# Performance work log

Hardware: AMD Instinct MI355X
Metric: run time of the kernel (lower is better)

The kernel has to match this reference:

```python
import jax, jax.numpy as jnp
import numpy as np
from jax import lax

B, S, D, H, TMAX = 8, 512, 256, 4, 20
DH = D // H
LAMBDA = 1e-3
V_TH = 1.0


def setup_inputs() -> dict:
    key = jax.random.key(0)
    ks = jax.random.split(key, 10)
    sc = lambda n: 1.0 / np.sqrt(n)
    f32 = jnp.float32
    return {
        "x": jax.random.normal(ks[0], (B, S, D), f32),
        "Wq": (jax.random.normal(ks[1], (D, D), f32) * sc(D)),
        "Wk": (jax.random.normal(ks[2], (D, D), f32) * sc(D)),
        "Wv": (jax.random.normal(ks[3], (D, D), f32) * sc(D)),
        "Wo": (jax.random.normal(ks[4], (D, D), f32) * sc(D)),
        "bo": jnp.zeros((D,), f32),
        "Wg1": (jax.random.normal(ks[5], (D, 32), f32) * sc(D)),
        "bg1": jnp.zeros((32,), f32),
        "Wg2": (jax.random.normal(ks[6], (32, 1), f32) * sc(32)),
        "bg2": jnp.zeros((1,), f32),
        "alpha_q": jnp.asarray(np.exp(-1 / 5.0), f32),
        "beta_q": jnp.asarray(np.exp(-1 / 20.0), f32),
        "alpha_k": jnp.asarray(np.exp(-1 / 5.0), f32),
        "beta_k": jnp.asarray(np.exp(-1 / 20.0), f32),
        "alpha_v": jnp.asarray(np.exp(-1 / 5.0), f32),
        "beta_v": jnp.asarray(np.exp(-1 / 20.0), f32),
    }


def _lif_spikes(x, alpha, beta, Ti):
    """LIF recurrence with CONSTANT input x per step, sequential only over T.
    x: [B,S,D], Ti: [B,S] int. Returns spikes [B,S,TMAX,D], zeroed for t >= Ti
    (equivalent to the original per-(b,s) loop that only runs Ti steps,
    since the recurrence is causal)."""
    zeros = jnp.zeros_like(x)
    tmask = jnp.arange(TMAX)

    def step(carry, t):
        v, i = carry
        i = alpha * i + x
        v = beta * v + i
        spk = (v >= V_TH).astype(x.dtype)
        v = v * (1.0 - spk)  # v_reset = 0
        spk_out = spk * (t < Ti).astype(x.dtype)[..., None]
        return (v, i), spk_out

    _, spks = lax.scan(step, (zeros, zeros), tmask)
    return jnp.moveaxis(spks, 0, 2)  # [B,S,T,D]


def reference(x, Wq, Wk, Wv, Wo, bo, Wg1, bg1, Wg2, bg2,
              alpha_q, beta_q, alpha_k, beta_k, alpha_v, beta_v):
    q = x @ Wq
    k = x @ Wk
    v = x @ Wv
    # adaptive window gate -> Ti in [1, TMAX]
    gate = jax.nn.sigmoid(jax.nn.relu(x @ Wg1 + bg1) @ Wg2 + bg2)[..., 0]  # [B,S]
    Ti = jnp.clip(jnp.ceil(gate * TMAX), 1, TMAX).astype(jnp.int32)
    q_spk = _lif_spikes(q, alpha_q, beta_q, Ti)  # [B,S,T,D]
    k_spk = _lif_spikes(k, alpha_k, beta_k, Ti)
    v_spk = _lif_spikes(v, alpha_v, beta_v, Ti)
    qh = q_spk.reshape(B, S, TMAX, H, DH)
    kh = k_spk.reshape(B, S, TMAX, H, DH)
    vh = v_spk.reshape(B, S, TMAX, H, DH)
    scale = DH ** -0.5
    Sraw = jnp.einsum('bithd,bjthd->bhij', qh, kh) * scale  # [B,H,S,S]
    W = jax.nn.softmax(Sraw, axis=-1)
    v_mean = vh.mean(axis=2)  # [B,S,H,DH] (mean over full T, zeros beyond Ti)
    out = jnp.einsum('bhij,bjhd->bihd', W, v_mean).reshape(B, S, D)
    out = out @ Wo + bo
    reg = LAMBDA * Ti.astype(jnp.float32).mean()
    return out, reg, Ti, W
```

## Files before the change

kernel.cpp:

```cpp
#include <hip/hip_runtime.h>
#include <hip/hip_bf16.h>

typedef unsigned long long u64;
typedef unsigned short u16;
typedef __attribute__((ext_vector_type(8))) short short8;
typedef __attribute__((ext_vector_type(4))) float float4_t;

#define BB 8
#define SS 512
#define DD 256
#define HH 4
#define TT 20
#define BS (BB*SS)

#define REG_OFF (BS*DD)
#define TI_OFF  (REG_OFF+1)
#define W_OFF   (TI_OFF+BS)

static __device__ __forceinline__ u16 f2bf(float f) {
    __hip_bfloat16 h = __float2bfloat16(f);
    return *reinterpret_cast<u16*>(&h);
}

__global__ __launch_bounds__(256) void k_gate(
    const float* __restrict__ x,
    const float* __restrict__ Wg1, const float* __restrict__ bg1,
    const float* __restrict__ Wg2, const float* __restrict__ bg2,
    float* __restrict__ ti_out)
{
    __shared__ float xl[8][DD];
    const int tid  = threadIdx.x;
    const int tok0 = blockIdx.x * 8;
    #pragma unroll
    for (int m = 0; m < 8; ++m) xl[m][tid] = x[(size_t)(tok0+m)*DD + tid];
    __syncthreads();

    const int tok = tid >> 5, c = tid & 31;
    float acc = bg1[c];
    #pragma unroll 4
    for (int r = 0; r < DD; ++r) acc += xl[tok][r] * Wg1[r*32 + c];
    float hrelu = acc > 0.f ? acc : 0.f;
    float term  = hrelu * Wg2[c];
    #pragma unroll
    for (int msk = 16; msk >= 1; msk >>= 1) term += __shfl_xor(term, msk, 64);
    if (c == 0) {
        float g  = term + bg2[0];
        float sg = 1.f / (1.f + expf(-g));
        int ti = (int)ceilf(sg * (float)TT);
        ti = ti < 1 ? 1 : (ti > TT ? TT : ti);
        ti_out[tok0 + tok] = (float)ti;
    }
}

__global__ __launch_bounds__(256) void k_proj_lif(
    const float* __restrict__ x, const float* __restrict__ Wq,
    const float* __restrict__ Wk, const float* __restrict__ Wv,
    const float* __restrict__ aq, const float* __restrict__ bq_,
    const float* __restrict__ ak, const float* __restrict__ bk_,
    const float* __restrict__ av, const float* __restrict__ bv_,
    const float* __restrict__ ti_in,
    u64* __restrict__ qpack, u64* __restrict__ kpack,
    u16* __restrict__ vmb)
{
    __shared__ float xl[DD][8];
    __shared__ int til[8];
    const int tid  = threadIdx.x;
    const int proj = blockIdx.y;
    const int tok0 = blockIdx.x * 8;

    #pragma unroll
    for (int m = 0; m < 8; ++m) xl[tid][m] = x[(size_t)(tok0+m)*DD + tid];
    if (tid < 8) til[tid] = (int)ti_in[tok0 + tid];
    __syncthreads();

    const float* W    = proj == 0 ? Wq  : (proj == 1 ? Wk  : Wv);
    const float alpha = proj == 0 ? *aq : (proj == 1 ? *ak : *av);
    const float beta  = proj == 0 ? *bq_: (proj == 1 ? *bk_: *bv_);

    float acc[8] = {0,0,0,0,0,0,0,0};
    #pragma unroll 4
    for (int r = 0; r < DD; ++r) {
        float w = W[r*DD + tid];
        float4_t x0 = *reinterpret_cast<const float4_t*>(&xl[r][0]);
        float4_t x1 = *reinterpret_cast<const float4_t*>(&xl[r][4]);
        acc[0] += x0.x*w; acc[1] += x0.y*w; acc[2] += x0.z*w; acc[3] += x0.w*w;
        acc[4] += x1.x*w; acc[5] += x1.y*w; acc[6] += x1.z*w; acc[7] += x1.w*w;
    }

    const int lane = tid & 63;
    const int h    = tid >> 6;
    u64* pack = (proj == 0) ? qpack : kpack;

    if (proj < 2) {
        for (int i = 0; i < 8; ++i) {
            int ti = til[i];
            float vv = 0.f, cur = 0.f;
            u64 myw = 0ull;
            #pragma unroll
            for (int t = 0; t < TT; ++t) {
                cur = alpha*cur + acc[i];
                vv  = beta*vv + cur;
                bool s = (vv >= 1.f);
                u64 bal = __ballot(s);
                if (s) vv = 0.f;
                if (lane == t && t < ti) myw = bal;
            }
            if (lane < TT) pack[((size_t)(tok0+i)*HH + h)*TT + lane] = myw;
        }
    } else {
        for (int i = 0; i < 8; ++i) {
            int ti = til[i];
            float vv = 0.f, cur = 0.f;
            float cnt = 0.f;
            #pragma unroll
            for (int t = 0; t < TT; ++t) {
                cur = alpha*cur + acc[i];
                vv  = beta*vv + cur;
                bool s = (vv >= 1.f);
                if (s) { vv = 0.f; if (t < ti) cnt += 1.f; }
            }
            vmb[(size_t)(tok0+i)*DD + tid] = f2bf(cnt * 0.05f);
        }
    }
}

__global__ __launch_bounds__(256) void k_reg(const float* __restrict__ ti, float* __restrict__ reg)
{
    __shared__ float ps[4];
    int tid = threadIdx.x;
    float s = 0.f;
    for (int m = 0; m < 16; ++m) s += ti[m*256 + tid];
    for (int msk = 32; msk >= 1; msk >>= 1) s += __shfl_xor(s, msk, 64);
    if ((tid & 63) == 0) ps[tid >> 6] = s;
    __syncthreads();
    if (tid == 0) reg[0] = 1e-3f * (ps[0]+ps[1]+ps[2]+ps[3]) / 4096.f;
}

__global__ __launch_bounds__(256) void k_attn(
    const u64* __restrict__ qpack, const u64* __restrict__ kpack,
    const u16* __restrict__ vmb,
    float* __restrict__ Wout, float* __restrict__ attn)
{
    __shared__ u64 ql[16][TT];
    __shared__ __align__(16) u16 CP[16*SS];
    const int tid  = threadIdx.x;
    const int tile = blockIdx.x & 31;
    const int h    = (blockIdx.x >> 5) & 3;
    const int b    = blockIdx.x >> 7;
    const int i0   = tile * 16;
    const int lane = tid & 63, wv = tid >> 6;

    for (int idx = tid; idx < 16*TT; idx += 256) {
        int i = idx / TT, t = idx - i*TT;
        ql[i][t] = qpack[((size_t)(b*SS + i0 + i)*HH + h)*TT + t];
    }

    u64 kr0[TT], kr1[TT];
    {
        const u64* kp0 = &kpack[((size_t)(b*SS + tid      )*HH + h)*TT];
        const u64* kp1 = &kpack[((size_t)(b*SS + tid + 256)*HH + h)*TT];
        #pragma unroll
        for (int t = 0; t < TT; ++t) { kr0[t] = kp0[t]; kr1[t] = kp1[t]; }
    }
    __syncthreads();

    for (int i = 0; i < 16; ++i) {
        int c0 = 0, c1 = 0;
        #pragma unroll
        for (int t = 0; t < TT; ++t) {
            u64 q = ql[i][t];
            c0 += __popcll(q & kr0[t]);
            c1 += __popcll(q & kr1[t]);
        }
        CP[i*SS + tid]       = (u16)c0;
        CP[i*SS + tid + 256] = (u16)c1;
    }
    __syncthreads();

    for (int rr = 0; rr < 4; ++rr) {
        const int i = wv*4 + rr;
        float sv[8];
        float m = -1e30f;
        #pragma unroll
        for (int k2 = 0; k2 < 8; ++k2) {
            sv[k2] = (float)CP[i*SS + lane + 64*k2] * 0.125f;
            m = fmaxf(m, sv[k2]);
        }
        #pragma unroll
        for (int msk = 32; msk >= 1; msk >>= 1) m = fmaxf(m, __shfl_xor(m, msk, 64));
        float sum = 0.f;
        #pragma unroll
        for (int k2 = 0; k2 < 8; ++k2) { sv[k2] = expf(sv[k2] - m); sum += sv[k2]; }
        #pragma unroll
        for (int msk = 32; msk >= 1; msk >>= 1) sum += __shfl_xor(sum, msk, 64);
        float inv = 1.f / sum;
        size_t wbase = ((size_t)((b*HH + h)*SS) + i0 + i) * SS;
        #pragma unroll
        for (int k2 = 0; k2 < 8; ++k2) {
            int j = lane + 64*k2;
            float wval = sv[k2] * inv;
            Wout[wbase + j] = wval;
            CP[(i*SS + j) ^ ((i & 7) << 3)] = f2bf(wval);
        }
    }
    __syncthreads();

    const int n0 = wv * 16;
    const int mr = lane & 15;
    const int g  = lane >> 4;
    float4_t acc = {0.f, 0.f, 0.f, 0.f};
    const u16* vb_base = vmb + (size_t)b*SS*DD + h*64 + n0 + mr;
    for (int ks = 0; ks < 16; ++ks) {
        int k = ks*32 + g*8;
        int aidx = (mr*SS + k) ^ ((mr & 7) << 3);
        short8 a = *reinterpret_cast<const short8*>(&CP[aidx]);
        union { u16 u[8]; short8 v; } bu;
        const u16* vb = vb_base + (size_t)k*DD;
        #pragma unroll
        for (int j = 0; j < 8; ++j) bu.u[j] = vb[(size_t)j*DD];
        acc = __builtin_amdgcn_mfma_f32_16x16x32_bf16(a, bu.v, acc, 0, 0, 0);
    }
    #pragma unroll
    for (int r = 0; r < 4; ++r) {
        int row = g*4 + r;
        attn[(size_t)(b*SS + i0 + row)*DD + h*64 + n0 + mr] = acc[r];
    }
}

__global__ __launch_bounds__(256) void k_outproj(
    const float* __restrict__ attn, const float* __restrict__ Wo,
    const float* __restrict__ bo, float* __restrict__ out)
{
    __shared__ float al[DD][8];
    const int tid  = threadIdx.x;
    const int tok0 = blockIdx.x * 8;
    #pragma unroll
    for (int m = 0; m < 8; ++m) al[tid][m] = attn[(size_t)(tok0+m)*DD + tid];
    __syncthreads();
    float acc[8] = {0,0,0,0,0,0,0,0};
    #pragma unroll 4
    for (int r = 0; r < DD; ++r) {
        float w = Wo[r*DD + tid];
        float4_t a0 = *reinterpret_cast<const float4_t*>(&al[r][0]);
        float4_t a1 = *reinterpret_cast<const float4_t*>(&al[r][4]);
        acc[0] += a0.x*w; acc[1] += a0.y*w; acc[2] += a0.z*w; acc[3] += a0.w*w;
        acc[4] += a1.x*w; acc[5] += a1.y*w; acc[6] += a1.z*w; acc[7] += a1.w*w;
    }
    float bb = bo[tid];
    #pragma unroll
    for (int i = 0; i < 8; ++i) out[(size_t)(tok0+i)*DD + tid] = acc[i] + bb;
}

extern "C" void kernel_launch(void* const* d_in, const int* in_sizes, int n_in,
                              void* d_out, int out_size, void* d_ws, size_t ws_size,
                              hipStream_t stream)
{
    (void)in_sizes; (void)n_in; (void)out_size; (void)ws_size;
    const float* x   = (const float*)d_in[0];
    const float* Wq  = (const float*)d_in[1];
    const float* Wk  = (const float*)d_in[2];
    const float* Wv  = (const float*)d_in[3];
    const float* Wo  = (const float*)d_in[4];
    const float* bo  = (const float*)d_in[5];
    const float* Wg1 = (const float*)d_in[6];
    const float* bg1 = (const float*)d_in[7];
    const float* Wg2 = (const float*)d_in[8];
    const float* bg2 = (const float*)d_in[9];
    const float* aq  = (const float*)d_in[10];
    const float* bq  = (const float*)d_in[11];
    const float* ak  = (const float*)d_in[12];
    const float* bk  = (const float*)d_in[13];
    const float* av  = (const float*)d_in[14];
    const float* bv  = (const float*)d_in[15];
    float* out = (float*)d_out;

    u64* qp = (u64*)d_ws;
    u64* kp = qp + (size_t)BS*HH*TT;
    u16* vmb = (u16*)(kp + (size_t)BS*HH*TT);
    float* attnbuf = (float*)(vmb + (size_t)BS*DD);

    k_gate<<<512, 256, 0, stream>>>(x, Wg1, bg1, Wg2, bg2, out + TI_OFF);
    k_reg<<<1, 256, 0, stream>>>(out + TI_OFF, out + REG_OFF);
    dim3 gproj(512, 3);
    k_proj_lif<<<gproj, 256, 0, stream>>>(x, Wq, Wk, Wv,
        aq, bq, ak, bk, av, bv, out + TI_OFF, qp, kp, vmb);
    k_attn<<<1024, 256, 0, stream>>>(qp, kp, vmb, out + W_OFF, attnbuf);
    k_outproj<<<512, 256, 0, stream>>>(attnbuf, Wo, bo, out);
}
```

Before: 127.1 us.

## Split-K projections with float4 weight loads, fuse reg reduction, reshape gate kernel

The projection and output-projection GEMV kernels now split the reduction dimension across the four waves. Each thread loads float4 weight columns and computes four outputs, and the partial sums are combined through a shared-memory union buffer. The gate kernel drops the shared staging and assigns one wave per token, with each half-wave covering half of D and combined by a shuffle. The separate reg reduction kernel is folded into block 0 of the output projection, removing one launch. In exchange the GEMVs pay an extra shared-memory reduction with two more barriers.

```diff
diff --git a/kernel.cpp b/kernel.cpp
--- a/kernel.cpp
+++ b/kernel.cpp
@@ -28,27 +28,33 @@
     const float* __restrict__ Wg2, const float* __restrict__ bg2,
     float* __restrict__ ti_out)
 {
-    __shared__ float xl[8][DD];
     const int tid  = threadIdx.x;
-    const int tok0 = blockIdx.x * 8;
-    #pragma unroll
-    for (int m = 0; m < 8; ++m) xl[m][tid] = x[(size_t)(tok0+m)*DD + tid];
-    __syncthreads();
-
-    const int tok = tid >> 5, c = tid & 31;
-    float acc = bg1[c];
+    const int tok  = blockIdx.x * 4 + (tid >> 6);
+    const int lane = tid & 63;
+    const int c    = lane & 31;
+    const int half = lane >> 5;
+
+    const float* xr = x + (size_t)tok*DD + half*128;
+    const float* wg = Wg1 + (size_t)half*128*32 + c;
+    float acc = 0.f;
     #pragma unroll 4
-    for (int r = 0; r < DD; ++r) acc += xl[tok][r] * Wg1[r*32 + c];
+    for (int i = 0; i < 32; ++i) {
+        float4_t xv = *reinterpret_cast<const float4_t*>(xr + i*4);
+        acc += xv.x * wg[(i*4+0)*32] + xv.y * wg[(i*4+1)*32]
+             + xv.z * wg[(i*4+2)*32] + xv.w * wg[(i*4+3)*32];
+    }
+    acc += __shfl_xor(acc, 32, 64);
+    acc += bg1[c];
     float hrelu = acc > 0.f ? acc : 0.f;
     float term  = hrelu * Wg2[c];
     #pragma unroll
     for (int msk = 16; msk >= 1; msk >>= 1) term += __shfl_xor(term, msk, 64);
-    if (c == 0) {
+    if (lane == 0) {
         float g  = term + bg2[0];
         float sg = 1.f / (1.f + expf(-g));
         int ti = (int)ceilf(sg * (float)TT);
         ti = ti < 1 ? 1 : (ti > TT ? TT : ti);
-        ti_out[tok0 + tok] = (float)ti;
+        ti_out[tok] = (float)ti;
     }
 }
 
@@ -62,14 +68,18 @@
     u64* __restrict__ qpack, u64* __restrict__ kpack,
     u16* __restrict__ vmb)
 {
-    __shared__ float xl[DD][8];
+    __shared__ __align__(16) union {
+        float xt[DD][8];
+        float red[4][8][DD];
+    } sm;
     __shared__ int til[8];
     const int tid  = threadIdx.x;
     const int proj = blockIdx.y;
     const int tok0 = blockIdx.x * 8;
-
-    #pragma unroll
-    for (int m = 0; m < 8; ++m) xl[tid][m] = x[(size_t)(tok0+m)*DD + tid];
+    const int w = tid >> 6, l = tid & 63;
+
+    #pragma unroll
+    for (int m = 0; m < 8; ++m) sm.xt[tid][m] = x[(size_t)(tok0+m)*DD + tid];
     if (tid < 8) til[tid] = (int)ti_in[tok0 + tid];
     __syncthreads();
 
@@ -77,44 +87,58 @@
     const float alpha = proj == 0 ? *aq : (proj == 1 ? *ak : *av);
     const float beta  = proj == 0 ? *bq_: (proj == 1 ? *bk_: *bv_);
 
-    float acc[8] = {0,0,0,0,0,0,0,0};
+    float4_t a[8];
+    #pragma unroll
+    for (int i = 0; i < 8; ++i) a[i] = (float4_t){0.f, 0.f, 0.f, 0.f};
+
+    const float* Wp = W + (size_t)(w*64)*DD + l*4;
     #pragma unroll 4
-    for (int r = 0; r < DD; ++r) {
-        float w = W[r*DD + tid];
-        float4_t x0 = *reinterpret_cast<const float4_t*>(&xl[r][0]);
-        float4_t x1 = *reinterpret_cast<const float4_t*>(&xl[r][4]);
-        acc[0] += x0.x*w; acc[1] += x0.y*w; acc[2] += x0.z*w; acc[3] += x0.w*w;
-        acc[4] += x1.x*w; acc[5] += x1.y*w; acc[6] += x1.z*w; acc[7] += x1.w*w;
-    }
-
-    const int lane = tid & 63;
-    const int h    = tid >> 6;
-    u64* pack = (proj == 0) ? qpack : kpack;
-
+    for (int r0 = 0; r0 < 64; ++r0) {
+        float4_t wf = *reinterpret_cast<const float4_t*>(Wp + (size_t)r0*DD);
+        int r = (w << 6) + r0;
+        float4_t x0 = *reinterpret_cast<const float4_t*>(&sm.xt[r][0]);
+        float4_t x1 = *reinterpret_cast<const float4_t*>(&sm.xt[r][4]);
+        a[0] += wf*x0.x; a[1] += wf*x0.y; a[2] += wf*x0.z; a[3] += wf*x0.w;
+        a[4] += wf*x1.x; a[5] += wf*x1.y; a[6] += wf*x1.z; a[7] += wf*x1.w;
+    }
+    __syncthreads();
+    #pragma unroll
+    for (int i = 0; i < 8; ++i)
+        *reinterpret_cast<float4_t*>(&sm.red[w][i][l*4]) = a[i];
+    __syncthreads();
+
+    float val[8];
+    #pragma unroll
+    for (int i = 0; i < 8; ++i)
+        val[i] = (sm.red[0][i][tid] + sm.red[1][i][tid])
+               + (sm.red[2][i][tid] + sm.red[3][i][tid]);
+
+    const int h = w;
     if (proj < 2) {
+        u64* pack = (proj == 0) ? qpack : kpack;
         for (int i = 0; i < 8; ++i) {
-            int ti = til[i];
+            const int ti = til[i];
             float vv = 0.f, cur = 0.f;
             u64 myw = 0ull;
             #pragma unroll
             for (int t = 0; t < TT; ++t) {
-                cur = alpha*cur + acc[i];
+                cur = alpha*cur + val[i];
                 vv  = beta*vv + cur;
                 bool s = (vv >= 1.f);
                 u64 bal = __ballot(s);
                 if (s) vv = 0.f;
-                if (lane == t && t < ti) myw = bal;
+                if (l == t && t < ti) myw = bal;
             }
-            if (lane < TT) pack[((size_t)(tok0+i)*HH + h)*TT + lane] = myw;
+            if (l < TT)
+                pack[((size_t)(tok0+i)*HH + h)*TT + l] = myw;
         }
     } else {
         for (int i = 0; i < 8; ++i) {
-            int ti = til[i];
-            float vv = 0.f, cur = 0.f;
-            float cnt = 0.f;
+            const int ti = til[i];
+            float vv = 0.f, cur = 0.f, cnt = 0.f;
             #pragma unroll
             for (int t = 0; t < TT; ++t) {
-                cur = alpha*cur + acc[i];
+                cur = alpha*cur + val[i];
                 vv  = beta*vv + cur;
                 bool s = (vv >= 1.f);
                 if (s) { vv = 0.f; if (t < ti) cnt += 1.f; }
@@ -122,18 +146,6 @@
             vmb[(size_t)(tok0+i)*DD + tid] = f2bf(cnt * 0.05f);
         }
     }
-}
-
-__global__ __launch_bounds__(256) void k_reg(const float* __restrict__ ti, float* __restrict__ reg)
-{
-    __shared__ float ps[4];
-    int tid = threadIdx.x;
-    float s = 0.f;
-    for (int m = 0; m < 16; ++m) s += ti[m*256 + tid];
-    for (int msk = 32; msk >= 1; msk >>= 1) s += __shfl_xor(s, msk, 64);
-    if ((tid & 63) == 0) ps[tid >> 6] = s;
-    __syncthreads();
-    if (tid == 0) reg[0] = 1e-3f * (ps[0]+ps[1]+ps[2]+ps[3]) / 4096.f;
 }
 
 __global__ __launch_bounds__(256) void k_attn(
@@ -229,26 +241,58 @@
 
 __global__ __launch_bounds__(256) void k_outproj(
     const float* __restrict__ attn, const float* __restrict__ Wo,
-    const float* __restrict__ bo, float* __restrict__ out)
-{
-    __shared__ float al[DD][8];
+    const float* __restrict__ bo, const float* __restrict__ ti,
+    float* __restrict__ out)
+{
+    __shared__ __align__(16) union {
+        float xt[DD][8];
+        float red[4][8][DD];
+    } sm;
+    __shared__ float ps[4];
     const int tid  = threadIdx.x;
     const int tok0 = blockIdx.x * 8;
-    #pragma unroll
-    for (int m = 0; m < 8; ++m) al[tid][m] = attn[(size_t)(tok0+m)*DD + tid];
-    __syncthreads();
-    float acc[8] = {0,0,0,0,0,0,0,0};
+    const int w = tid >> 6, l = tid & 63;
+
+    #pragma unroll
+    for (int m = 0; m < 8; ++m) sm.xt[tid][m] = attn[(size_t)(tok0+m)*DD + tid];
+    __syncthreads();
+
+    float4_t a[8];
+    #pragma unroll
+    for (int i = 0; i < 8; ++i) a[i] = (float4_t){0.f, 0.f, 0.f, 0.f};
+    const float* Wp = Wo + (size_t)(w*64)*DD + l*4;
     #pragma unroll 4
-    for (int r = 0; r < DD; ++r) {
-        float w = Wo[r*DD + tid];
-        float4_t a0 = *reinterpret_cast<const float4_t*>(&al[r][0]);
-        float4_t a1 = *reinterpret_cast<const float4_t*>(&al[r][4]);
-        acc[0] += a0.x*w; acc[1] += a0.y*w; acc[2] += a0.z*w; acc[3] += a0.w*w;
-        acc[4] += a1.x*w; acc[5] += a1.y*w; acc[6] += a1.z*w; acc[7] += a1.w*w;
-    }
+    for (int r0 = 0; r0 < 64; ++r0) {
+        float4_t wf = *reinterpret_cast<const float4_t*>(Wp + (size_t)r0*DD);
+        int r = (w << 6) + r0;
+        float4_t x0 = *reinterpret_cast<const float4_t*>(&sm.xt[r][0]);
+        float4_t x1 = *reinterpret_cast<const float4_t*>(&sm.xt[r][4]);
+        a[0] += wf*x0.x; a[1] += wf*x0.y; a[2] += wf*x0.z; a[3] += wf*x0.w;
+        a[4] += wf*x1.x; a[5] += wf*x1.y; a[6] += wf*x1.z; a[7] += wf*x1.w;
+    }
+    __syncthreads();
+    #pragma unroll
+    for (int i = 0; i < 8; ++i)
+        *reinterpret_cast<float4_t*>(&sm.red[w][i][l*4]) = a[i];
+    __syncthreads();
+
     float bb = bo[tid];
     #pragma unroll
-    for (int i = 0; i < 8; ++i) out[(size_t)(tok0+i)*DD + tid] = acc[i] + bb;
+    for (int i = 0; i < 8; ++i) {
+        float v = (sm.red[0][i][tid] + sm.red[1][i][tid])
+                + (sm.red[2][i][tid] + sm.red[3][i][tid]);
+        out[(size_t)(tok0+i)*DD + tid] = v + bb;
+    }
+
+    if (blockIdx.x == 0) {
+        float s = 0.f;
+        for (int m = 0; m < 16; ++m) s += ti[m*256 + tid];
+        #pragma unroll
+        for (int msk = 32; msk >= 1; msk >>= 1) s += __shfl_xor(s, msk, 64);
+        if ((tid & 63) == 0) ps[tid >> 6] = s;
+        __syncthreads();
+        if (tid == 0) out[REG_OFF] = 1e-3f * (ps[0]+ps[1]+ps[2]+ps[3]) / 4096.f;
+    }
 }
 
 extern "C" void kernel_launch(void* const* d_in, const int* in_sizes, int n_in,
@@ -279,11 +323,10 @@
     u16* vmb = (u16*)(kp + (size_t)BS*HH*TT);
     float* attnbuf = (float*)(vmb + (size_t)BS*DD);
 
-    k_gate<<<512, 256, 0, stream>>>(x, Wg1, bg1, Wg2, bg2, out + TI_OFF);
-    k_reg<<<1, 256, 0, stream>>>(out + TI_OFF, out + REG_OFF);
+    k_gate<<<1024, 256, 0, stream>>>(x, Wg1, bg1, Wg2, bg2, out + TI_OFF);
     dim3 gproj(512, 3);
     k_proj_lif<<<gproj, 256, 0, stream>>>(x, Wq, Wk, Wv,
         aq, bq, ak, bk, av, bv, out + TI_OFF, qp, kp, vmb);
     k_attn<<<1024, 256, 0, stream>>>(qp, kp, vmb, out + W_OFF, attnbuf);
-    k_outproj<<<512, 256, 0, stream>>>(attnbuf, Wo, bo, out);
-}
+    k_outproj<<<512, 256, 0, stream>>>(attnbuf, Wo, bo, out + TI_OFF, out);
+}
```

Result: faster. 102.9 us (-19.1%).
